# Kernel tuning notes

Hardware: AMD Instinct MI355X
Metric: run time of the kernel (lower is better)

Reference implementation:

```python
import jax, jax.numpy as jnp
import numpy as np

BATCH, SEQ, STATE, OBS, INP = 4096, 512, 16, 8, 4


def setup_inputs() -> dict:
    key = jax.random.key(0)
    ks = jax.random.split(key, 5)
    # scale A to spectral radius ~0.3 so the 512-step recursion is stable
    A = jax.random.normal(ks[0], (STATE, STATE), jnp.float32) * (0.3 / np.sqrt(STATE))
    B = jax.random.normal(ks[1], (STATE, INP), jnp.float32) * 0.1
    C = jax.random.normal(ks[2], (OBS, STATE), jnp.float32) * (1.0 / np.sqrt(STATE))
    Q = jnp.eye(STATE, dtype=jnp.float32)   # module default when Q is None
    R = jnp.eye(OBS, dtype=jnp.float32)     # module default when R is None
    x0 = jnp.zeros((STATE,), jnp.float32)   # module default initial_state_mean
    obs = jax.random.normal(ks[3], (BATCH, SEQ, OBS), jnp.float32)
    u = jax.random.normal(ks[4], (BATCH, SEQ, INP), jnp.float32)
    return {"obs": obs, "u": u, "A": A, "B": B, "C": C, "Q": Q, "R": R, "x0": x0}


def reference(obs, u, A, B, C, Q, R, x0):
    Bsz = obs.shape[0]
    S = A.shape[0]
    eyeS = jnp.eye(S, dtype=obs.dtype)
    x_init = jnp.broadcast_to(x0, (Bsz, S))                 # (B,S), P0 = I per module init
    P_init = jnp.broadcast_to(eyeS, (Bsz, S, S))

    def step(carry, inp):
        x, P = carry                                        # x:(B,S)  P:(B,S,S)
        u_k, z_k = inp                                      # (B,I), (B,O)
        # stage 1: prediction
        x_prior = x @ A.T + u_k @ B.T                       # (B,S)
        P_prior = A @ P @ A.T + Q                           # (B,S,S)
        # stage 2: measurement update
        Smat = C @ P_prior @ C.T + R                        # (B,O,O) innovation covariance
        K = P_prior @ C.T @ jnp.linalg.inv(Smat)            # (B,S,O)
        innov = z_k - x_prior @ C.T                         # (B,O)
        x_post = x_prior + jnp.einsum('bso,bo->bs', K, innov)
        P_post = (eyeS - K @ C) @ P_prior                   # (B,S,S)
        return (x_post, P_post), x_post

    inp_seq = (jnp.swapaxes(u, 0, 1), jnp.swapaxes(obs, 0, 1))  # time-major for scan
    _, xs = jax.lax.scan(step, (x_init, P_init), inp_seq)       # xs: (T,B,S)
    return jnp.swapaxes(xs, 0, 1)                               # (B,T,S) == states_est[:,1:,:]
```

## Files before the change

kernel.cpp:

```cpp
#include <hip/hip_runtime.h>
#include <hip/hip_bf16.h>

#define SEQ   512
#define BATCH 4096
#define NS    16
#define NO    8
#define NI    4
#define NK    12
#define CH    16
#define CL    (SEQ/CH)
#define CW    16

__device__ float g_gains[NK * 448];
__device__ int   g_isf32_data;
__device__ float g_x0[NS];

static __device__ __forceinline__ float bf2f_us(unsigned short v) {
    unsigned int u = ((unsigned int)v) << 16;
    return __uint_as_float(u);
}

__global__ __launch_bounds__(256) void riccati_kernel(
        const void* __restrict__ Ap, const void* __restrict__ Bp,
        const void* __restrict__ Cp, const void* __restrict__ Qp,
        const void* __restrict__ Rp, const void* __restrict__ x0p,
        const void* __restrict__ obsp) {
    __shared__ float A[NS*NS], Bm[NS*NI], Cm[NO*NS], Q[NS*NS], R[NO*NO];
    __shared__ float P[NS*NS], AP[NS*NS], Pp[NS*NS], CP[NO*NS];
    __shared__ float G[NO*2*NO], PCt[NS*NO], K[NS*NO];
    __shared__ float CA[NO*NS], CB[NO*NI], Pn[NS*NS];
    __shared__ int sflag_p, sflag_d;

    const int t = threadIdx.x;
    const int i = t >> 4, j = t & 15;

    if (t == 0) { sflag_p = 0; sflag_d = 0; }
    __syncthreads();
    {
        float v = fabsf(bf2f_us(((const unsigned short*)Ap)[t]));
        if (!(v < 16.0f)) sflag_p = 1;
        const unsigned short* oh = (const unsigned short*)obsp;
        for (int s = 0; s < 8; ++s) {
            float w = fabsf(bf2f_us(oh[t + 256*s]));
            if (!(w < 16.0f)) sflag_d = 1;
        }
    }
    __syncthreads();
    const bool f32p = (sflag_p != 0);
    if (t == 0) g_isf32_data = (sflag_d != 0) ? 1 : 0;

    auto ld = [&](const void* p, int idx) -> float {
        return f32p ? ((const float*)p)[idx]
                    : bf2f_us(((const unsigned short*)p)[idx]);
    };

    A[t] = ld(Ap, t);  Q[t] = ld(Qp, t);
    if (t < NS*NI) Bm[t] = ld(Bp, t);
    if (t < NO*NS) Cm[t] = ld(Cp, t);
    if (t < NO*NO) R[t]  = ld(Rp, t);
    if (t < NS)    g_x0[t] = ld(x0p, t);
    P[t] = (i == j) ? 1.0f : 0.0f;
    __syncthreads();

    if (i < NO) {
        float acc = 0.f;
        for (int l = 0; l < NS; ++l) acc += Cm[i*NS+l] * A[l*NS+j];
        CA[i*NS+j] = acc;
        if (j < NI) {
            float a2 = 0.f;
            for (int l = 0; l < NS; ++l) a2 += Cm[i*NS+l] * Bm[l*NI+j];
            CB[i*NI+j] = a2;
        }
    }
    __syncthreads();

    for (int k = 0; k < NK; ++k) {
        {
            float acc = 0.f;
            for (int l = 0; l < NS; ++l) acc += A[i*NS+l] * P[l*NS+j];
            AP[i*NS+j] = acc;
        }
        __syncthreads();
        {
            float acc = Q[i*NS+j];
            for (int l = 0; l < NS; ++l) acc += AP[i*NS+l] * A[j*NS+l];
            Pp[i*NS+j] = acc;
        }
        __syncthreads();
        if (i < NO) {
            float acc = 0.f;
            for (int l = 0; l < NS; ++l) acc += Cm[i*NS+l] * Pp[l*NS+j];
            CP[i*NS+j] = acc;
        }
        __syncthreads();
        if (i < NO) {
            if (j < NO) {
                float acc = R[i*NO+j];
                for (int l = 0; l < NS; ++l) acc += CP[i*NS+l] * Cm[j*NS+l];
                G[i*2*NO + j] = acc;
            } else {
                G[i*2*NO + j] = ((j - NO) == i) ? 1.0f : 0.0f;
            }
        }
        __syncthreads();
        for (int p = 0; p < NO; ++p) {
            float gij = 0.f, gpj = 0.f, gip = 0.f, piv = 1.f;
            if (i < NO) {
                piv = G[p*2*NO + p];
                gpj = G[p*2*NO + j];
                gip = G[i*2*NO + p];
                gij = G[i*2*NO + j];
            }
            __syncthreads();
            if (i < NO) {
                float r = gpj / piv;
                G[i*2*NO + j] = (i == p) ? r : (gij - gip * r);
            }
            __syncthreads();
        }
        if (j < NO) {
            float acc = 0.f;
            for (int l = 0; l < NS; ++l) acc += Pp[i*NS+l] * Cm[j*NS+l];
            PCt[i*NO+j] = acc;
        }
        __syncthreads();
        if (j < NO) {
            float acc = 0.f;
            for (int l = 0; l < NO; ++l) acc += PCt[i*NO+l] * G[l*2*NO + NO + j];
            K[i*NO+j] = acc;
        }
        __syncthreads();
        float* outp = g_gains + k * 448;
        {
            float acc = A[i*NS+j];
            for (int l = 0; l < NO; ++l) acc -= K[i*NO+l] * CA[l*NS+j];
            outp[i*NS+j] = acc;
        }
        if (j < NI) {
            float acc = Bm[i*NI+j];
            for (int l = 0; l < NO; ++l) acc -= K[i*NO+l] * CB[l*NI+j];
            outp[256 + i*NI+j] = acc;
        }
        if (j < NO) outp[320 + i*NO+j] = K[i*NO+j];
        {
            float acc = Pp[i*NS+j];
            for (int l = 0; l < NO; ++l) acc -= K[i*NO+l] * CP[l*NS+j];
            Pn[i*NS+j] = acc;
        }
        __syncthreads();
        P[i*NS+j] = Pn[i*NS+j];
        __syncthreads();
    }
}

template<bool F32>
static __device__ __forceinline__ void run_filter(
        const void* __restrict__ obsv, const void* __restrict__ uv,
        float* __restrict__ out, int c, int b) {
    const int cL = c * CL;
    const int k0 = (c == 0) ? 0 : (cL - CW);
    const int kend = cL + CL;

    float x[NS];
#pragma unroll
    for (int s = 0; s < NS; ++s) x[s] = (c == 0) ? g_x0[s] : 0.0f;

    float* op = out + (size_t)b * SEQ * NS;

    const float*          upf = (const float*)uv   + (size_t)b * SEQ * NI;
    const float*          zpf = (const float*)obsv + (size_t)b * SEQ * NO;
    const unsigned short* upb = (const unsigned short*)uv   + (size_t)b * SEQ * NI;
    const unsigned short* zpb = (const unsigned short*)obsv + (size_t)b * SEQ * NO;

    float4 uf, zf0, zf1;
    uint2 ub; uint4 zb;
    if (F32) {
        uf  = *(const float4*)(upf + (size_t)k0 * NI);
        zf0 = *(const float4*)(zpf + (size_t)k0 * NO);
        zf1 = *(const float4*)(zpf + (size_t)k0 * NO + 4);
    } else {
        ub = *(const uint2*)(upb + (size_t)k0 * NI);
        zb = *(const uint4*)(zpb + (size_t)k0 * NO);
    }

    for (int k = k0; k < kend; ++k) {
        float uu[NI], zz[NO];
        if (F32) {
            uu[0]=uf.x; uu[1]=uf.y; uu[2]=uf.z; uu[3]=uf.w;
            zz[0]=zf0.x; zz[1]=zf0.y; zz[2]=zf0.z; zz[3]=zf0.w;
            zz[4]=zf1.x; zz[5]=zf1.y; zz[6]=zf1.z; zz[7]=zf1.w;
            if (k + 1 < kend) {
                uf  = *(const float4*)(upf + (size_t)(k+1) * NI);
                zf0 = *(const float4*)(zpf + (size_t)(k+1) * NO);
                zf1 = *(const float4*)(zpf + (size_t)(k+1) * NO + 4);
            }
        } else {
            const uint2 uc = ub; const uint4 zc = zb;
            if (k + 1 < kend) {
                ub = *(const uint2*)(upb + (size_t)(k+1) * NI);
                zb = *(const uint4*)(zpb + (size_t)(k+1) * NO);
            }
            uu[0] = bf2f_us(uc.x & 0xffffu); uu[1] = bf2f_us(uc.x >> 16);
            uu[2] = bf2f_us(uc.y & 0xffffu); uu[3] = bf2f_us(uc.y >> 16);
            zz[0] = bf2f_us(zc.x & 0xffffu); zz[1] = bf2f_us(zc.x >> 16);
            zz[2] = bf2f_us(zc.y & 0xffffu); zz[3] = bf2f_us(zc.y >> 16);
            zz[4] = bf2f_us(zc.z & 0xffffu); zz[5] = bf2f_us(zc.z >> 16);
            zz[6] = bf2f_us(zc.w & 0xffffu); zz[7] = bf2f_us(zc.w >> 16);
        }

        const int idx = (k < NK) ? k : (NK - 1);
        const float4* G = (const float4*)(g_gains + (size_t)idx * 448);

        float xn[NS];
#pragma unroll
        for (int r = 0; r < NS; ++r) {
            float4 m0 = G[r*4 + 0], m1 = G[r*4 + 1], m2 = G[r*4 + 2], m3 = G[r*4 + 3];
            float acc;
            acc  = m0.x*x[0]  + m0.y*x[1]  + m0.z*x[2]  + m0.w*x[3];
            acc += m1.x*x[4]  + m1.y*x[5]  + m1.z*x[6]  + m1.w*x[7];
            acc += m2.x*x[8]  + m2.y*x[9]  + m2.z*x[10] + m2.w*x[11];
            acc += m3.x*x[12] + m3.y*x[13] + m3.z*x[14] + m3.w*x[15];
            float4 nv = G[64 + r];
            acc += nv.x*uu[0] + nv.y*uu[1] + nv.z*uu[2] + nv.w*uu[3];
            float4 k0v = G[80 + r*2], k1v = G[80 + r*2 + 1];
            acc += k0v.x*zz[0] + k0v.y*zz[1] + k0v.z*zz[2] + k0v.w*zz[3];
            acc += k1v.x*zz[4] + k1v.y*zz[5] + k1v.z*zz[6] + k1v.w*zz[7];
            xn[r] = acc;
        }
#pragma unroll
        for (int r = 0; r < NS; ++r) x[r] = xn[r];

        if (k >= cL) {
            float4* dst = (float4*)(op + (size_t)k * NS);
            dst[0] = make_float4(x[0],  x[1],  x[2],  x[3]);
            dst[1] = make_float4(x[4],  x[5],  x[6],  x[7]);
            dst[2] = make_float4(x[8],  x[9],  x[10], x[11]);
            dst[3] = make_float4(x[12], x[13], x[14], x[15]);
        }
    }
}

__global__ __launch_bounds__(256) void filter_kernel(
        const void* __restrict__ obs, const void* __restrict__ u,
        float* __restrict__ out) {
    const int c  = blockIdx.x / (BATCH/256);
    const int bg = blockIdx.x % (BATCH/256);
    const int b  = bg * 256 + threadIdx.x;
    if (g_isf32_data) run_filter<true >(obs, u, out, c, b);
    else              run_filter<false>(obs, u, out, c, b);
}

extern "C" void kernel_launch(void* const* d_in, const int* in_sizes, int n_in,
                              void* d_out, int out_size, void* d_ws, size_t ws_size,
                              hipStream_t stream) {
    const void* obs = d_in[0];
    const void* u   = d_in[1];
    const void* A   = d_in[2];
    const void* B   = d_in[3];
    const void* C   = d_in[4];
    const void* Q   = d_in[5];
    const void* R   = d_in[6];
    const void* x0  = d_in[7];
    float* out = (float*)d_out;

    riccati_kernel<<<1, 256, 0, stream>>>(A, B, C, Q, R, x0, obs);
    filter_kernel<<<dim3(CH * (BATCH/256)), dim3(256), 0, stream>>>(obs, u, out);
}
```

Before: 362.9 us.

## Split each batch filter across four lanes with DPP state exchange and register gains

Each batch element's 16-dim state update is now spread over four lanes. Every lane owns four state rows, keeps its slice of the gain matrices in registers, and gets the other lanes' state through quad DPP rotations. This gives four times more threads and removes per-step uniform gain reloads. It also double-buffers the input prefetch two steps ahead, drops the bf16/f32 runtime detection in favour of assuming fp32 inputs, and shrinks the Riccati kernel to one wavefront. The risks are more register pressure and the loss of bf16 input support.

```diff
diff --git a/kernel.cpp b/kernel.cpp
--- a/kernel.cpp
+++ b/kernel.cpp
@@ -12,257 +12,224 @@
 #define CW    16
 
 __device__ float g_gains[NK * 448];
-__device__ int   g_isf32_data;
 __device__ float g_x0[NS];
 
-static __device__ __forceinline__ float bf2f_us(unsigned short v) {
-    unsigned int u = ((unsigned int)v) << 16;
-    return __uint_as_float(u);
-}
-
-__global__ __launch_bounds__(256) void riccati_kernel(
-        const void* __restrict__ Ap, const void* __restrict__ Bp,
-        const void* __restrict__ Cp, const void* __restrict__ Qp,
-        const void* __restrict__ Rp, const void* __restrict__ x0p,
-        const void* __restrict__ obsp) {
-    __shared__ float A[NS*NS], Bm[NS*NI], Cm[NO*NS], Q[NS*NS], R[NO*NO];
-    __shared__ float P[NS*NS], AP[NS*NS], Pp[NS*NS], CP[NO*NS];
-    __shared__ float G[NO*2*NO], PCt[NS*NO], K[NS*NO];
-    __shared__ float CA[NO*NS], CB[NO*NI], Pn[NS*NS];
-    __shared__ int sflag_p, sflag_d;
-
+__global__ __launch_bounds__(64) void riccati_kernel(
+        const float* __restrict__ Apt, const float* __restrict__ Bpt,
+        const float* __restrict__ Cpt, const float* __restrict__ Qpt,
+        const float* __restrict__ Rpt, const float* __restrict__ x0pt) {
+    __shared__ float A[256], Bm[64], Cm[128], Q[256], R[64];
+    __shared__ float P[256], AP[256], Pp[256], CP[128];
+    __shared__ float G[128], PCt[128], K[128], CA[128], CB[32], Pn[256];
     const int t = threadIdx.x;
-    const int i = t >> 4, j = t & 15;
-
-    if (t == 0) { sflag_p = 0; sflag_d = 0; }
+
+    for (int idx = t; idx < 256; idx += 64) {
+        A[idx] = Apt[idx]; Q[idx] = Qpt[idx];
+        P[idx] = ((idx >> 4) == (idx & 15)) ? 1.0f : 0.0f;
+    }
+    Bm[t] = Bpt[t]; R[t] = Rpt[t];
+    for (int idx = t; idx < 128; idx += 64) Cm[idx] = Cpt[idx];
+    if (t < 16) g_x0[t] = x0pt[t];
     __syncthreads();
+
+    for (int idx = t; idx < 128; idx += 64) {
+        int i = idx >> 4, j = idx & 15; float acc = 0.f;
+        for (int l = 0; l < 16; ++l) acc += Cm[i*16+l] * A[l*16+j];
+        CA[idx] = acc;
+    }
+    if (t < 32) {
+        int i = t >> 2, j = t & 3; float acc = 0.f;
+        for (int l = 0; l < 16; ++l) acc += Cm[i*16+l] * Bm[l*4+j];
+        CB[t] = acc;
+    }
+    __syncthreads();
+
+    for (int k = 0; k < NK; ++k) {
+        for (int idx = t; idx < 256; idx += 64) {
+            int i = idx >> 4, j = idx & 15; float a = 0.f;
+            for (int l = 0; l < 16; ++l) a += A[i*16+l] * P[l*16+j];
+            AP[idx] = a;
+        }
+        __syncthreads();
+        for (int idx = t; idx < 256; idx += 64) {
+            int i = idx >> 4, j = idx & 15; float a = Q[idx];
+            for (int l = 0; l < 16; ++l) a += AP[i*16+l] * A[j*16+l];
+            Pp[idx] = a;
+        }
+        __syncthreads();
+        for (int idx = t; idx < 128; idx += 64) {
+            int i = idx >> 4, j = idx & 15; float a = 0.f;
+            for (int l = 0; l < 16; ++l) a += Cm[i*16+l] * Pp[l*16+j];
+            CP[idx] = a;
+        }
+        __syncthreads();
+        for (int idx = t; idx < 128; idx += 64) {
+            int i = idx >> 4, j = idx & 15; float a;
+            if (j < 8) { a = R[i*8+j]; for (int l = 0; l < 16; ++l) a += CP[i*16+l] * Cm[j*16+l]; }
+            else a = ((j - 8) == i) ? 1.0f : 0.0f;
+            G[idx] = a;
+        }
+        __syncthreads();
+        for (int p = 0; p < 8; ++p) {
+            const int i0 = t >> 4, j0 = t & 15, i1 = i0 + 4;
+            float piv = G[p*16+p];
+            float gp  = G[p*16+j0];
+            float gi0 = G[i0*16+p], gv0 = G[i0*16+j0];
+            float gi1 = G[i1*16+p], gv1 = G[i1*16+j0];
+            __syncthreads();
+            float r = gp / piv;
+            G[i0*16+j0] = (i0 == p) ? r : (gv0 - gi0 * r);
+            G[i1*16+j0] = (i1 == p) ? r : (gv1 - gi1 * r);
+            __syncthreads();
+        }
+        for (int idx = t; idx < 128; idx += 64) {
+            int i = idx >> 3, j = idx & 7; float a = 0.f;
+            for (int l = 0; l < 16; ++l) a += Pp[i*16+l] * Cm[j*16+l];
+            PCt[idx] = a;
+        }
+        __syncthreads();
+        for (int idx = t; idx < 128; idx += 64) {
+            int i = idx >> 3, j = idx & 7; float a = 0.f;
+            for (int l = 0; l < 8; ++l) a += PCt[i*8+l] * G[l*16+8+j];
+            K[idx] = a;
+        }
+        __syncthreads();
+        float* outp = g_gains + k * 448;
+        for (int idx = t; idx < 256; idx += 64) {
+            int i = idx >> 4, j = idx & 15; float a = A[idx];
+            for (int l = 0; l < 8; ++l) a -= K[i*8+l] * CA[l*16+j];
+            outp[idx] = a;
+        }
+        {   int i = t >> 2, j = t & 3; float a = Bm[t];
+            for (int l = 0; l < 8; ++l) a -= K[i*8+l] * CB[l*4+j];
+            outp[256 + t] = a;
+        }
+        for (int idx = t; idx < 128; idx += 64) outp[320 + idx] = K[idx];
+        for (int idx = t; idx < 256; idx += 64) {
+            int i = idx >> 4, j = idx & 15; float a = Pp[idx];
+            for (int l = 0; l < 8; ++l) a -= K[i*8+l] * CP[l*16+j];
+            Pn[idx] = a;
+        }
+        __syncthreads();
+        for (int idx = t; idx < 256; idx += 64) P[idx] = Pn[idx];
+        __syncthreads();
+    }
+}
+
+template<int CTRL>
+static __device__ __forceinline__ float qrot(float v) {
+    return __int_as_float(__builtin_amdgcn_mov_dpp(__float_as_int(v), CTRL, 0xf, 0xf, true));
+}
+
+__global__ __launch_bounds__(256) void filter_kernel(
+        const float* __restrict__ obs, const float* __restrict__ u,
+        float* __restrict__ out) {
+    const int t    = threadIdx.x;
+    const int lane = t & 3;
+    const int c    = blockIdx.x >> 6;
+    const int bg   = blockIdx.x & 63;
+    const int b    = bg * 64 + (t >> 2);
+    const int cL   = c * CL;
+    const int k0   = (c == 0) ? 0 : (cL - CW);
+    const int kend = cL + CL;
+
+    float4 Mv[4][4], Nv[4], Kv[4][2];
+    auto load_gains = [&](int idx) {
+        const float* g = g_gains + idx * 448;
+        const int row0 = 4 * lane;
+#pragma unroll
+        for (int i = 0; i < 4; ++i) {
+            const float* mrow = g + (row0 + i) * 16;
+#pragma unroll
+            for (int r = 0; r < 4; ++r)
+                Mv[i][r] = *(const float4*)(mrow + 4 * ((lane + r) & 3));
+            Nv[i]    = *(const float4*)(g + 256 + (row0 + i) * 4);
+            Kv[i][0] = *(const float4*)(g + 320 + (row0 + i) * 8);
+            Kv[i][1] = *(const float4*)(g + 320 + (row0 + i) * 8 + 4);
+        }
+    };
+    if (k0 >= NK) load_gains(NK - 1);
+
+    float x[4];
+#pragma unroll
+    for (int i = 0; i < 4; ++i) x[i] = (c == 0) ? g_x0[4*lane + i] : 0.0f;
+
+    const float* up = u   + (size_t)b * SEQ * NI;
+    const float* zp = obs + (size_t)b * SEQ * NO;
+    float*       op = out + (size_t)b * SEQ * NS + 4 * lane;
+
+    float4 ub[2], z0b[2], z1b[2];
     {
-        float v = fabsf(bf2f_us(((const unsigned short*)Ap)[t]));
-        if (!(v < 16.0f)) sflag_p = 1;
-        const unsigned short* oh = (const unsigned short*)obsp;
-        for (int s = 0; s < 8; ++s) {
-            float w = fabsf(bf2f_us(oh[t + 256*s]));
-            if (!(w < 16.0f)) sflag_d = 1;
-        }
-    }
-    __syncthreads();
-    const bool f32p = (sflag_p != 0);
-    if (t == 0) g_isf32_data = (sflag_d != 0) ? 1 : 0;
-
-    auto ld = [&](const void* p, int idx) -> float {
-        return f32p ? ((const float*)p)[idx]
-                    : bf2f_us(((const unsigned short*)p)[idx]);
-    };
-
-    A[t] = ld(Ap, t);  Q[t] = ld(Qp, t);
-    if (t < NS*NI) Bm[t] = ld(Bp, t);
-    if (t < NO*NS) Cm[t] = ld(Cp, t);
-    if (t < NO*NO) R[t]  = ld(Rp, t);
-    if (t < NS)    g_x0[t] = ld(x0p, t);
-    P[t] = (i == j) ? 1.0f : 0.0f;
-    __syncthreads();
-
-    if (i < NO) {
-        float acc = 0.f;
-        for (int l = 0; l < NS; ++l) acc += Cm[i*NS+l] * A[l*NS+j];
-        CA[i*NS+j] = acc;
-        if (j < NI) {
-            float a2 = 0.f;
-            for (int l = 0; l < NS; ++l) a2 += Cm[i*NS+l] * Bm[l*NI+j];
-            CB[i*NI+j] = a2;
-        }
-    }
-    __syncthreads();
-
-    for (int k = 0; k < NK; ++k) {
-        {
-            float acc = 0.f;
-            for (int l = 0; l < NS; ++l) acc += A[i*NS+l] * P[l*NS+j];
-            AP[i*NS+j] = acc;
-        }
-        __syncthreads();
-        {
-            float acc = Q[i*NS+j];
-            for (int l = 0; l < NS; ++l) acc += AP[i*NS+l] * A[j*NS+l];
-            Pp[i*NS+j] = acc;
-        }
-        __syncthreads();
-        if (i < NO) {
-            float acc = 0.f;
-            for (int l = 0; l < NS; ++l) acc += Cm[i*NS+l] * Pp[l*NS+j];
-            CP[i*NS+j] = acc;
-        }
-        __syncthreads();
-        if (i < NO) {
-            if (j < NO) {
-                float acc = R[i*NO+j];
-                for (int l = 0; l < NS; ++l) acc += CP[i*NS+l] * Cm[j*NS+l];
-                G[i*2*NO + j] = acc;
-            } else {
-                G[i*2*NO + j] = ((j - NO) == i) ? 1.0f : 0.0f;
-            }
-        }
-        __syncthreads();
-        for (int p = 0; p < NO; ++p) {
-            float gij = 0.f, gpj = 0.f, gip = 0.f, piv = 1.f;
-            if (i < NO) {
-                piv = G[p*2*NO + p];
-                gpj = G[p*2*NO + j];
-                gip = G[i*2*NO + p];
-                gij = G[i*2*NO + j];
-            }
-            __syncthreads();
-            if (i < NO) {
-                float r = gpj / piv;
-                G[i*2*NO + j] = (i == p) ? r : (gij - gip * r);
-            }
-            __syncthreads();
-        }
-        if (j < NO) {
-            float acc = 0.f;
-            for (int l = 0; l < NS; ++l) acc += Pp[i*NS+l] * Cm[j*NS+l];
-            PCt[i*NO+j] = acc;
-        }
-        __syncthreads();
-        if (j < NO) {
-            float acc = 0.f;
-            for (int l = 0; l < NO; ++l) acc += PCt[i*NO+l] * G[l*2*NO + NO + j];
-            K[i*NO+j] = acc;
-        }
-        __syncthreads();
-        float* outp = g_gains + k * 448;
-        {
-            float acc = A[i*NS+j];
-            for (int l = 0; l < NO; ++l) acc -= K[i*NO+l] * CA[l*NS+j];
-            outp[i*NS+j] = acc;
-        }
-        if (j < NI) {
-            float acc = Bm[i*NI+j];
-            for (int l = 0; l < NO; ++l) acc -= K[i*NO+l] * CB[l*NI+j];
-            outp[256 + i*NI+j] = acc;
-        }
-        if (j < NO) outp[320 + i*NO+j] = K[i*NO+j];
-        {
-            float acc = Pp[i*NS+j];
-            for (int l = 0; l < NO; ++l) acc -= K[i*NO+l] * CP[l*NS+j];
-            Pn[i*NS+j] = acc;
-        }
-        __syncthreads();
-        P[i*NS+j] = Pn[i*NS+j];
-        __syncthreads();
-    }
-}
-
-template<bool F32>
-static __device__ __forceinline__ void run_filter(
-        const void* __restrict__ obsv, const void* __restrict__ uv,
-        float* __restrict__ out, int c, int b) {
-    const int cL = c * CL;
-    const int k0 = (c == 0) ? 0 : (cL - CW);
-    const int kend = cL + CL;
-
-    float x[NS];
-#pragma unroll
-    for (int s = 0; s < NS; ++s) x[s] = (c == 0) ? g_x0[s] : 0.0f;
-
-    float* op = out + (size_t)b * SEQ * NS;
-
-    const float*          upf = (const float*)uv   + (size_t)b * SEQ * NI;
-    const float*          zpf = (const float*)obsv + (size_t)b * SEQ * NO;
-    const unsigned short* upb = (const unsigned short*)uv   + (size_t)b * SEQ * NI;
-    const unsigned short* zpb = (const unsigned short*)obsv + (size_t)b * SEQ * NO;
-
-    float4 uf, zf0, zf1;
-    uint2 ub; uint4 zb;
-    if (F32) {
-        uf  = *(const float4*)(upf + (size_t)k0 * NI);
-        zf0 = *(const float4*)(zpf + (size_t)k0 * NO);
-        zf1 = *(const float4*)(zpf + (size_t)k0 * NO + 4);
-    } else {
-        ub = *(const uint2*)(upb + (size_t)k0 * NI);
-        zb = *(const uint4*)(zpb + (size_t)k0 * NO);
-    }
-
+        int ka = k0, kb = (k0 + 1 < kend) ? k0 + 1 : kend - 1;
+        ub[0]  = *(const float4*)(up + ka * NI);
+        z0b[0] = *(const float4*)(zp + ka * NO);
+        z1b[0] = *(const float4*)(zp + ka * NO + 4);
+        ub[1]  = *(const float4*)(up + kb * NI);
+        z0b[1] = *(const float4*)(zp + kb * NO);
+        z1b[1] = *(const float4*)(zp + kb * NO + 4);
+    }
+
+#pragma unroll 2
     for (int k = k0; k < kend; ++k) {
-        float uu[NI], zz[NO];
-        if (F32) {
-            uu[0]=uf.x; uu[1]=uf.y; uu[2]=uf.z; uu[3]=uf.w;
-            zz[0]=zf0.x; zz[1]=zf0.y; zz[2]=zf0.z; zz[3]=zf0.w;
-            zz[4]=zf1.x; zz[5]=zf1.y; zz[6]=zf1.z; zz[7]=zf1.w;
-            if (k + 1 < kend) {
-                uf  = *(const float4*)(upf + (size_t)(k+1) * NI);
-                zf0 = *(const float4*)(zpf + (size_t)(k+1) * NO);
-                zf1 = *(const float4*)(zpf + (size_t)(k+1) * NO + 4);
-            }
-        } else {
-            const uint2 uc = ub; const uint4 zc = zb;
-            if (k + 1 < kend) {
-                ub = *(const uint2*)(upb + (size_t)(k+1) * NI);
-                zb = *(const uint4*)(zpb + (size_t)(k+1) * NO);
-            }
-            uu[0] = bf2f_us(uc.x & 0xffffu); uu[1] = bf2f_us(uc.x >> 16);
-            uu[2] = bf2f_us(uc.y & 0xffffu); uu[3] = bf2f_us(uc.y >> 16);
-            zz[0] = bf2f_us(zc.x & 0xffffu); zz[1] = bf2f_us(zc.x >> 16);
-            zz[2] = bf2f_us(zc.y & 0xffffu); zz[3] = bf2f_us(zc.y >> 16);
-            zz[4] = bf2f_us(zc.z & 0xffffu); zz[5] = bf2f_us(zc.z >> 16);
-            zz[6] = bf2f_us(zc.w & 0xffffu); zz[7] = bf2f_us(zc.w >> 16);
-        }
-
-        const int idx = (k < NK) ? k : (NK - 1);
-        const float4* G = (const float4*)(g_gains + (size_t)idx * 448);
-
-        float xn[NS];
-#pragma unroll
-        for (int r = 0; r < NS; ++r) {
-            float4 m0 = G[r*4 + 0], m1 = G[r*4 + 1], m2 = G[r*4 + 2], m3 = G[r*4 + 3];
-            float acc;
-            acc  = m0.x*x[0]  + m0.y*x[1]  + m0.z*x[2]  + m0.w*x[3];
-            acc += m1.x*x[4]  + m1.y*x[5]  + m1.z*x[6]  + m1.w*x[7];
-            acc += m2.x*x[8]  + m2.y*x[9]  + m2.z*x[10] + m2.w*x[11];
-            acc += m3.x*x[12] + m3.y*x[13] + m3.z*x[14] + m3.w*x[15];
-            float4 nv = G[64 + r];
-            acc += nv.x*uu[0] + nv.y*uu[1] + nv.z*uu[2] + nv.w*uu[3];
-            float4 k0v = G[80 + r*2], k1v = G[80 + r*2 + 1];
-            acc += k0v.x*zz[0] + k0v.y*zz[1] + k0v.z*zz[2] + k0v.w*zz[3];
-            acc += k1v.x*zz[4] + k1v.y*zz[5] + k1v.z*zz[6] + k1v.w*zz[7];
-            xn[r] = acc;
-        }
-#pragma unroll
-        for (int r = 0; r < NS; ++r) x[r] = xn[r];
-
-        if (k >= cL) {
-            float4* dst = (float4*)(op + (size_t)k * NS);
-            dst[0] = make_float4(x[0],  x[1],  x[2],  x[3]);
-            dst[1] = make_float4(x[4],  x[5],  x[6],  x[7]);
-            dst[2] = make_float4(x[8],  x[9],  x[10], x[11]);
-            dst[3] = make_float4(x[12], x[13], x[14], x[15]);
-        }
-    }
-}
-
-__global__ __launch_bounds__(256) void filter_kernel(
-        const void* __restrict__ obs, const void* __restrict__ u,
-        float* __restrict__ out) {
-    const int c  = blockIdx.x / (BATCH/256);
-    const int bg = blockIdx.x % (BATCH/256);
-    const int b  = bg * 256 + threadIdx.x;
-    if (g_isf32_data) run_filter<true >(obs, u, out, c, b);
-    else              run_filter<false>(obs, u, out, c, b);
+        const int p = (k - k0) & 1;
+        if (k < NK) load_gains(k);
+        float4 uc = ub[p], zc0 = z0b[p], zc1 = z1b[p];
+        {
+            int kf = (k + 2 < kend) ? k + 2 : kend - 1;
+            ub[p]  = *(const float4*)(up + kf * NI);
+            z0b[p] = *(const float4*)(zp + kf * NO);
+            z1b[p] = *(const float4*)(zp + kf * NO + 4);
+        }
+        float acc[4];
+#pragma unroll
+        for (int i = 0; i < 4; ++i) {
+            acc[i]  = Nv[i].x*uc.x  + Nv[i].y*uc.y  + Nv[i].z*uc.z  + Nv[i].w*uc.w;
+            acc[i] += Kv[i][0].x*zc0.x + Kv[i][0].y*zc0.y + Kv[i][0].z*zc0.z + Kv[i][0].w*zc0.w;
+            acc[i] += Kv[i][1].x*zc1.x + Kv[i][1].y*zc1.y + Kv[i][1].z*zc1.z + Kv[i][1].w*zc1.w;
+            acc[i] += Mv[i][0].x*x[0] + Mv[i][0].y*x[1] + Mv[i][0].z*x[2] + Mv[i][0].w*x[3];
+        }
+        {
+            float y0 = qrot<0x39>(x[0]), y1 = qrot<0x39>(x[1]),
+                  y2 = qrot<0x39>(x[2]), y3 = qrot<0x39>(x[3]);
+#pragma unroll
+            for (int i = 0; i < 4; ++i)
+                acc[i] += Mv[i][1].x*y0 + Mv[i][1].y*y1 + Mv[i][1].z*y2 + Mv[i][1].w*y3;
+        }
+        {
+            float y0 = qrot<0x4E>(x[0]), y1 = qrot<0x4E>(x[1]),
+                  y2 = qrot<0x4E>(x[2]), y3 = qrot<0x4E>(x[3]);
+#pragma unroll
+            for (int i = 0; i < 4; ++i)
+                acc[i] += Mv[i][2].x*y0 + Mv[i][2].y*y1 + Mv[i][2].z*y2 + Mv[i][2].w*y3;
+        }
+        {
+            float y0 = qrot<0x93>(x[0]), y1 = qrot<0x93>(x[1]),
+                  y2 = qrot<0x93>(x[2]), y3 = qrot<0x93>(x[3]);
+#pragma unroll
+            for (int i = 0; i < 4; ++i)
+                acc[i] += Mv[i][3].x*y0 + Mv[i][3].y*y1 + Mv[i][3].z*y2 + Mv[i][3].w*y3;
+        }
+#pragma unroll
+        for (int i = 0; i < 4; ++i) x[i] = acc[i];
+
+        if (k >= cL)
+            *(float4*)(op + (size_t)k * NS) = make_float4(x[0], x[1], x[2], x[3]);
+    }
 }
 
 extern "C" void kernel_launch(void* const* d_in, const int* in_sizes, int n_in,
                               void* d_out, int out_size, void* d_ws, size_t ws_size,
                               hipStream_t stream) {
-    const void* obs = d_in[0];
-    const void* u   = d_in[1];
-    const void* A   = d_in[2];
-    const void* B   = d_in[3];
-    const void* C   = d_in[4];
-    const void* Q   = d_in[5];
-    const void* R   = d_in[6];
-    const void* x0  = d_in[7];
+    const float* obs = (const float*)d_in[0];
+    const float* u   = (const float*)d_in[1];
+    const float* A   = (const float*)d_in[2];
+    const float* B   = (const float*)d_in[3];
+    const float* C   = (const float*)d_in[4];
+    const float* Q   = (const float*)d_in[5];
+    const float* R   = (const float*)d_in[6];
+    const float* x0  = (const float*)d_in[7];
     float* out = (float*)d_out;
 
-    riccati_kernel<<<1, 256, 0, stream>>>(A, B, C, Q, R, x0, obs);
-    filter_kernel<<<dim3(CH * (BATCH/256)), dim3(256), 0, stream>>>(obs, u, out);
-}
+    riccati_kernel<<<1, 64, 0, stream>>>(A, B, C, Q, R, x0);
+    filter_kernel<<<dim3(CH * (BATCH*4/256)), dim3(256), 0, stream>>>(obs, u, out);
+}
```

Measured after the change: 381.0 us. +5.0%, slower.
